# Kernel optimization log

Hardware: AMD Instinct MI355X
Metric: run time of the kernel (lower is better)

The kernel has to match this reference:

```python
import jax, jax.numpy as jnp
import numpy as np

NINP = 1024
NHID = 1024
BATCH = 16384
EPS = 1e-5


def _ln(x, g, b):
    mu = jnp.mean(x, axis=-1, keepdims=True)
    var = jnp.mean(jnp.square(x - mu), axis=-1, keepdims=True)
    return (x - mu) * jax.lax.rsqrt(var + EPS) * g + b


def setup_inputs() -> dict:
    key = jax.random.key(0)
    ks = jax.random.split(key, 12)
    s_i = 1.0 / np.sqrt(NINP)
    s_h = 1.0 / np.sqrt(NHID)
    return {
        "inp": jax.random.normal(ks[0], (BATCH, NINP), jnp.float32),
        "hidden": jax.random.normal(ks[1], (BATCH, NHID), jnp.float32),
        "W_i2gate": jax.random.uniform(ks[2], (3 * NHID, NINP), jnp.float32, -s_i, s_i),
        "b_i2gate": jnp.zeros((3 * NHID,), jnp.float32),
        "W_h2gate": jax.random.uniform(ks[3], (3 * NHID, NHID), jnp.float32, -s_h, s_h),
        "b_h2gate": jnp.zeros((3 * NHID,), jnp.float32),
        "W_i2i": jax.random.uniform(ks[4], (NHID, NINP), jnp.float32, -s_i, s_i),
        "b_i2i": jnp.zeros((NHID,), jnp.float32),
        "W_i2h": jax.random.uniform(ks[5], (NHID, NINP), jnp.float32, -s_i, s_i),
        "b_i2h": jnp.zeros((NHID,), jnp.float32),
        "W_h2h": jax.random.uniform(ks[6], (NHID, NHID), jnp.float32, -s_h, s_h),
        "b_h2h": jnp.zeros((NHID,), jnp.float32),
        "g_ig": jnp.ones((3 * NHID,), jnp.float32),
        "be_ig": jnp.zeros((3 * NHID,), jnp.float32),
        "g_hg": jnp.ones((3 * NHID,), jnp.float32),
        "be_hg": jnp.zeros((3 * NHID,), jnp.float32),
        "g_ii": jnp.ones((NHID,), jnp.float32),
        "be_ii": jnp.zeros((NHID,), jnp.float32),
        "g_ih": jnp.ones((NHID,), jnp.float32),
        "be_ih": jnp.zeros((NHID,), jnp.float32),
        "g_hh": jnp.ones((NHID,), jnp.float32),
        "be_hh": jnp.zeros((NHID,), jnp.float32),
    }


def reference(inp, hidden, W_i2gate, b_i2gate, W_h2gate, b_h2gate,
              W_i2i, b_i2i, W_i2h, b_i2h, W_h2h, b_h2h,
              g_ig, be_ig, g_hg, be_hg, g_ii, be_ii,
              g_ih, be_ih, g_hh, be_hh):
    gate = jax.nn.sigmoid(
        _ln(inp @ W_i2gate.T + b_i2gate, g_ig, be_ig)
        + _ln(hidden @ W_h2gate.T + b_h2gate, g_hg, be_hg))
    r, z, g = jnp.split(gate, 3, axis=-1)
    Hx = _ln(inp @ W_i2i.T + b_i2i, g_ii, be_ii)
    xh = _ln(inp @ W_i2h.T + b_i2h, g_ih, be_ih)
    hh = _ln(hidden @ W_h2h.T + b_h2h, g_hh, be_hh)
    hidden_m = jnp.tanh((1.0 - r) * xh + r * hh)
    return ((1.0 - z) * hidden + z * hidden_m) * (1.0 - g) + g * Hx
```

## Files before the change

kernel.cpp:

```cpp
#include <hip/hip_runtime.h>

typedef __bf16 bf16_t;
typedef bf16_t bf16x8 __attribute__((ext_vector_type(8)));
typedef bf16_t bf16x4 __attribute__((ext_vector_type(4)));
typedef float f32x4 __attribute__((ext_vector_type(4)));

#define BATCH 16384
#define KDIM  1024
#define NCOLS 9216

#define BMg 256
#define BNg 256
#define BKg 64
#define NTg (KDIM / BKg)
#define NBN (NCOLS / BNg)

__global__ __launch_bounds__(256)
void cast_all(const float* __restrict__ Wig, const float* __restrict__ Wii,
              const float* __restrict__ Wih, const float* __restrict__ Whg,
              const float* __restrict__ Whh,
              const float* __restrict__ big, const float* __restrict__ bii,
              const float* __restrict__ bih, const float* __restrict__ bhg,
              const float* __restrict__ bhh,
              const float* __restrict__ inp, const float* __restrict__ hid,
              bf16_t* __restrict__ Wcat, float* __restrict__ bcat,
              bf16_t* __restrict__ inpb, bf16_t* __restrict__ hidb,
              int nact_units, int ntot)
{
  int u = blockIdx.x * 256 + threadIdx.x;
  if (u >= ntot) return;

  if (u < 2359296) {
    const float* src; int off;
    if      (u < 786432)  { src = Wig; off = u; }
    else if (u < 1048576) { src = Wii; off = u - 786432; }
    else if (u < 1310720) { src = Wih; off = u - 1048576; }
    else if (u < 2097152) { src = Whg; off = u - 1310720; }
    else                  { src = Whh; off = u - 2097152; }
    float4 v = reinterpret_cast<const float4*>(src)[off];
    bf16x4 o;
    o[0] = (bf16_t)v.x; o[1] = (bf16_t)v.y; o[2] = (bf16_t)v.z; o[3] = (bf16_t)v.w;
    reinterpret_cast<bf16x4*>(Wcat)[u] = o;
  } else if (u < 2361600) {
    int bu = u - 2359296;
    int i = bu * 4;
    const float* src; int off;
    if      (i < 3072) { src = big; off = i; }
    else if (i < 4096) { src = bii; off = i - 3072; }
    else if (i < 5120) { src = bih; off = i - 4096; }
    else if (i < 8192) { src = bhg; off = i - 5120; }
    else               { src = bhh; off = i - 8192; }
    reinterpret_cast<float4*>(bcat)[bu] = *reinterpret_cast<const float4*>(src + off);
  } else {
    int au = u - 2361600;
    const float* src; bf16_t* dst; int off;
    if (au < nact_units) { src = inp; dst = inpb; off = au; }
    else                 { src = hid; dst = hidb; off = au - nact_units; }
    float4 v = reinterpret_cast<const float4*>(src)[off];
    bf16x4 o;
    o[0] = (bf16_t)v.x; o[1] = (bf16_t)v.y; o[2] = (bf16_t)v.z; o[3] = (bf16_t)v.w;
    reinterpret_cast<bf16x4*>(dst)[off] = o;
  }
}

__global__ __launch_bounds__(256)
void cast_acts(const float* __restrict__ inp, const float* __restrict__ hid,
               bf16_t* __restrict__ inpb, bf16_t* __restrict__ hidb, int n4) {
  int i = blockIdx.x * 256 + threadIdx.x;
  if (i >= 2 * n4) return;
  const float* src = (i < n4) ? inp : hid;
  bf16_t* dst = (i < n4) ? inpb : hidb;
  int off = (i < n4) ? i : i - n4;
  float4 v = reinterpret_cast<const float4*>(src)[off];
  bf16x4 o;
  o[0] = (bf16_t)v.x; o[1] = (bf16_t)v.y; o[2] = (bf16_t)v.z; o[3] = (bf16_t)v.w;
  reinterpret_cast<bf16x4*>(dst)[off] = o;
}

__global__ __launch_bounds__(512, 2)
void gemm_preln(const bf16_t* __restrict__ inpb, const bf16_t* __restrict__ hidb,
                const bf16_t* __restrict__ Wcat, const float* __restrict__ bcat,
                bf16_t* __restrict__ preLN, int nbm)
{
  __shared__ alignas(16) char lds_raw[131072];

  const int tid  = threadIdx.x;
  const int wid  = tid >> 6;
  const int lane = tid & 63;
  const int fr   = lane & 15;
  const int kg   = lane >> 4;
  const int wr   = wid >> 2;
  const int wc   = wid & 3;

  const int nwg = nbm * NBN;
  int orig = blockIdx.x;
  int q_ = nwg >> 3, r_ = nwg & 7, xcd = orig & 7, idx = orig >> 3;
  int wg = (xcd < r_ ? xcd * (q_ + 1) : r_ * (q_ + 1) + (xcd - r_) * q_) + idx;
  const int bm = wg / NBN, bn = wg % NBN;
  const int row0 = bm * BMg, col0 = bn * BNg;
  const bf16_t* __restrict__ act = (col0 < 5120) ? inpb : hidb;
  const bf16_t* __restrict__ wgt = Wcat + (size_t)col0 * KDIM;

  const int r_st  = tid >> 2;
  const int k8_st = (tid & 3) ^ ((r_st >> 1) & 3);
  const bf16_t* pA = act + (size_t)(row0 + r_st) * KDIM + k8_st * 8;
  const bf16_t* pB = wgt + (size_t)r_st * KDIM + k8_st * 8;

  auto stage_half = [&](int mat, int h, int T) {
    const bf16_t* s = (mat ? pB : pA) + ((size_t)h * 128) * KDIM + T * BKg;
    char* d = lds_raw + ((T & 1) << 16) + (mat << 15) + (h << 14) + (wid << 10);
    __builtin_amdgcn_global_load_lds(
        (const __attribute__((address_space(1))) unsigned int*)s,
        (__attribute__((address_space(3))) unsigned int*)d, 16, 0, 0);
    __builtin_amdgcn_global_load_lds(
        (const __attribute__((address_space(1))) unsigned int*)(s + 32),
        (__attribute__((address_space(3))) unsigned int*)(d + 8192), 16, 0, 0);
  };

  int offA[4][2], offB[2][2];
  #pragma unroll
  for (int m = 0; m < 4; ++m)
    #pragma unroll
    for (int ks = 0; ks < 2; ++ks) {
      const int rowA = wr * 64 + m * 16 + fr;
      offA[m][ks] = ks * 8192 + rowA * 64 + ((kg ^ ((rowA >> 1) & 3)) << 4);
    }
  #pragma unroll
  for (int n = 0; n < 2; ++n)
    #pragma unroll
    for (int ks = 0; ks < 2; ++ks) {
      const int rowB = wc * 32 + n * 16 + fr;
      offB[n][ks] = ks * 8192 + rowB * 64 + ((kg ^ ((rowB >> 1) & 3)) << 4);
    }

  f32x4 acc[2][4][2][2] = {};

  stage_half(0, 0, 0); stage_half(1, 0, 0);
  stage_half(0, 1, 0); stage_half(1, 1, 0);
  stage_half(0, 0, 1); stage_half(1, 0, 1);
  asm volatile("s_waitcnt vmcnt(4)" ::: "memory");
  __builtin_amdgcn_s_barrier();

  for (int T = 0; T < NTg; ++T) {
    const int bufo = (T & 1) << 16;
    bf16x8 a[4][2], b0[2][2], b1[2][2];

    #pragma unroll
    for (int m = 0; m < 4; ++m)
      #pragma unroll
      for (int ks = 0; ks < 2; ++ks)
        a[m][ks] = *(const bf16x8*)(lds_raw + bufo + offA[m][ks]);
    #pragma unroll
    for (int n = 0; n < 2; ++n)
      #pragma unroll
      for (int ks = 0; ks < 2; ++ks)
        b0[n][ks] = *(const bf16x8*)(lds_raw + bufo + 32768 + offB[n][ks]);
    if (T + 1 < NTg) stage_half(0, 1, T + 1);
    __builtin_amdgcn_s_barrier();
    asm volatile("s_waitcnt lgkmcnt(0)" ::: "memory");
    __builtin_amdgcn_sched_barrier(0);
    __builtin_amdgcn_s_setprio(1);
    #pragma unroll
    for (int m = 0; m < 4; ++m)
      #pragma unroll
      for (int n = 0; n < 2; ++n)
        #pragma unroll
        for (int ks = 0; ks < 2; ++ks)
          acc[0][m][0][n] = __builtin_amdgcn_mfma_f32_16x16x32_bf16(a[m][ks], b0[n][ks], acc[0][m][0][n], 0, 0, 0);
    __builtin_amdgcn_s_setprio(0);
    __builtin_amdgcn_s_barrier();

    #pragma unroll
    for (int n = 0; n < 2; ++n)
      #pragma unroll
      for (int ks = 0; ks < 2; ++ks)
        b1[n][ks] = *(const bf16x8*)(lds_raw + bufo + 32768 + 16384 + offB[n][ks]);
    if (T + 1 < NTg) stage_half(1, 1, T + 1);
    __builtin_amdgcn_s_barrier();
    asm volatile("s_waitcnt lgkmcnt(0)" ::: "memory");
    __builtin_amdgcn_sched_barrier(0);
    __builtin_amdgcn_s_setprio(1);
    #pragma unroll
    for (int m = 0; m < 4; ++m)
      #pragma unroll
      for (int n = 0; n < 2; ++n)
        #pragma unroll
        for (int ks = 0; ks < 2; ++ks)
          acc[0][m][1][n] = __builtin_amdgcn_mfma_f32_16x16x32_bf16(a[m][ks], b1[n][ks], acc[0][m][1][n], 0, 0, 0);
    __builtin_amdgcn_s_setprio(0);
    __builtin_amdgcn_s_barrier();

    #pragma unroll
    for (int m = 0; m < 4; ++m)
      #pragma unroll
      for (int ks = 0; ks < 2; ++ks)
        a[m][ks] = *(const bf16x8*)(lds_raw + bufo + 16384 + offA[m][ks]);
    if (T + 2 < NTg) stage_half(0, 0, T + 2);
    __builtin_amdgcn_s_barrier();
    asm volatile("s_waitcnt lgkmcnt(0)" ::: "memory");
    __builtin_amdgcn_sched_barrier(0);
    __builtin_amdgcn_s_setprio(1);
    #pragma unroll
    for (int m = 0; m < 4; ++m)
      #pragma unroll
      for (int n = 0; n < 2; ++n)
        #pragma unroll
        for (int ks = 0; ks < 2; ++ks)
          acc[1][m][1][n] = __builtin_amdgcn_mfma_f32_16x16x32_bf16(a[m][ks], b1[n][ks], acc[1][m][1][n], 0, 0, 0);
    __builtin_amdgcn_s_setprio(0);
    __builtin_amdgcn_s_barrier();

    if (T + 2 < NTg) stage_half(1, 0, T + 2);
    __builtin_amdgcn_s_barrier();
    __builtin_amdgcn_s_setprio(1);
    #pragma unroll
    for (int m = 0; m < 4; ++m)
      #pragma unroll
      for (int n = 0; n < 2; ++n)
        #pragma unroll
        for (int ks = 0; ks < 2; ++ks)
          acc[1][m][0][n] = __builtin_amdgcn_mfma_f32_16x16x32_bf16(a[m][ks], b0[n][ks], acc[1][m][0][n], 0, 0, 0);
    __builtin_amdgcn_s_setprio(0);

    if (T < NTg - 2) {
      asm volatile("s_waitcnt vmcnt(4)" ::: "memory");
      __builtin_amdgcn_s_barrier();
    } else if (T == NTg - 2) {
      asm volatile("s_waitcnt vmcnt(0)" ::: "memory");
      __builtin_amdgcn_s_barrier();
    }
  }

  #pragma unroll
  for (int qn_ = 0; qn_ < 2; ++qn_)
    #pragma unroll
    for (int n = 0; n < 2; ++n) {
      const int col = col0 + qn_ * 128 + wc * 32 + n * 16 + fr;
      const float bias = bcat[col];
      #pragma unroll
      for (int qm_ = 0; qm_ < 2; ++qm_)
        #pragma unroll
        for (int m = 0; m < 4; ++m) {
          const int rbase = row0 + qm_ * 128 + wr * 64 + m * 16 + kg * 4;
          #pragma unroll
          for (int j = 0; j < 4; ++j)
            preLN[(size_t)(rbase + j) * NCOLS + col] = (bf16_t)(acc[qm_][m][qn_][n][j] + bias);
        }
    }
}

__global__ __launch_bounds__(256)
void ln_combine(const bf16_t* __restrict__ preLN, const float* __restrict__ hidden,
                const float* __restrict__ g_ig, const float* __restrict__ be_ig,
                const float* __restrict__ g_hg, const float* __restrict__ be_hg,
                const float* __restrict__ g_ii, const float* __restrict__ be_ii,
                const float* __restrict__ g_ih, const float* __restrict__ be_ih,
                const float* __restrict__ g_hh, const float* __restrict__ be_hh,
                float* __restrict__ out, int crows)
{
  const int ln  = threadIdx.x & 63;
  const int row = blockIdx.x * 4 + (threadIdx.x >> 6);
  if (row >= crows) return;
  const bf16_t* __restrict__ src = preLN + (size_t)row * NCOLS;

  float s1[5] = {0.f,0.f,0.f,0.f,0.f}, s2[5] = {0.f,0.f,0.f,0.f,0.f};
  #pragma unroll
  for (int j = 0; j < 18; ++j) {
    const int sg = (j < 6) ? 0 : (j < 8) ? 1 : (j < 10) ? 2 : (j < 16) ? 3 : 4;
    bf16x8 v = *(const bf16x8*)(src + (size_t)(j * 64 + ln) * 8);
    #pragma unroll
    for (int t = 0; t < 8; ++t) {
      float f = (float)v[t];
      s1[sg] += f;
      s2[sg] += f * f;
    }
  }
  #pragma unroll
  for (int s = 0; s < 5; ++s)
    #pragma unroll
    for (int off = 32; off; off >>= 1) {
      s1[s] += __shfl_xor(s1[s], off);
      s2[s] += __shfl_xor(s2[s], off);
    }
  const float nn[5] = {3072.f, 1024.f, 1024.f, 3072.f, 1024.f};
  float mu[5], rs[5];
  #pragma unroll
  for (int s = 0; s < 5; ++s) {
    mu[s] = s1[s] / nn[s];
    rs[s] = rsqrtf(s2[s] / nn[s] - mu[s] * mu[s] + 1e-5f);
  }
  const float mu0 = mu[0], r0s = rs[0];
  const float mu1 = mu[1], r1s = rs[1];
  const float mu2 = mu[2], r2s = rs[2];
  const float mu3 = mu[3], r3s = rs[3];
  const float mu4 = mu[4], r4s = rs[4];

  const float* __restrict__ hrow = hidden + (size_t)row * 1024;
  float* __restrict__ orow = out + (size_t)row * 1024;
  #pragma unroll
  for (int p = 0; p < 4; ++p) {
    const int c = p * 256 + ln * 4;
    bf16x4 v_igr = *(const bf16x4*)&src[c];
    bf16x4 v_igz = *(const bf16x4*)&src[c + 1024];
    bf16x4 v_igg = *(const bf16x4*)&src[c + 2048];
    bf16x4 v_ii  = *(const bf16x4*)&src[c + 3072];
    bf16x4 v_ih  = *(const bf16x4*)&src[c + 4096];
    bf16x4 v_hgr = *(const bf16x4*)&src[c + 5120];
    bf16x4 v_hgz = *(const bf16x4*)&src[c + 6144];
    bf16x4 v_hgg = *(const bf16x4*)&src[c + 7168];
    bf16x4 v_hh  = *(const bf16x4*)&src[c + 8192];

    f32x4 Gr  = *(const f32x4*)&g_ig[c];        f32x4 Br  = *(const f32x4*)&be_ig[c];
    f32x4 Gz  = *(const f32x4*)&g_ig[c + 1024]; f32x4 Bz  = *(const f32x4*)&be_ig[c + 1024];
    f32x4 Gg  = *(const f32x4*)&g_ig[c + 2048]; f32x4 Bg  = *(const f32x4*)&be_ig[c + 2048];
    f32x4 Hr  = *(const f32x4*)&g_hg[c];        f32x4 Cr  = *(const f32x4*)&be_hg[c];
    f32x4 Hz  = *(const f32x4*)&g_hg[c + 1024]; f32x4 Cz  = *(const f32x4*)&be_hg[c + 1024];
    f32x4 Hg  = *(const f32x4*)&g_hg[c + 2048]; f32x4 Cg  = *(const f32x4*)&be_hg[c + 2048];
    f32x4 Gii = *(const f32x4*)&g_ii[c];        f32x4 Bii = *(const f32x4*)&be_ii[c];
    f32x4 Gih = *(const f32x4*)&g_ih[c];        f32x4 Bih = *(const f32x4*)&be_ih[c];
    f32x4 Ghh = *(const f32x4*)&g_hh[c];        f32x4 Bhh = *(const f32x4*)&be_hh[c];
    f32x4 hv  = *(const f32x4*)&hrow[c];

    f32x4 o;
    #pragma unroll
    for (int i = 0; i < 4; ++i) {
      float pr = ((float)v_igr[i] - mu0) * r0s * Gr[i] + Br[i]
               + ((float)v_hgr[i] - mu3) * r3s * Hr[i] + Cr[i];
      float pz = ((float)v_igz[i] - mu0) * r0s * Gz[i] + Bz[i]
               + ((float)v_hgz[i] - mu3) * r3s * Hz[i] + Cz[i];
      float pg = ((float)v_igg[i] - mu0) * r0s * Gg[i] + Bg[i]
               + ((float)v_hgg[i] - mu3) * r3s * Hg[i] + Cg[i];

      float rr = 1.f / (1.f + __expf(-pr));
      float zz = 1.f / (1.f + __expf(-pz));
      float gg = 1.f / (1.f + __expf(-pg));

      float Hx = ((float)v_ii[i] - mu1) * r1s * Gii[i] + Bii[i];
      float xh = ((float)v_ih[i] - mu2) * r2s * Gih[i] + Bih[i];
      float hh = ((float)v_hh[i] - mu4) * r4s * Ghh[i] + Bhh[i];

      float pre = (1.f - rr) * xh + rr * hh;
      float hm  = 1.f - 2.f / (1.f + __expf(2.f * pre));
      o[i] = ((1.f - zz) * hv[i] + zz * hm) * (1.f - gg) + gg * Hx;
    }
    *(f32x4*)&orow[c] = o;
  }
}

extern "C" void kernel_launch(void* const* d_in, const int* in_sizes, int n_in,
                              void* d_out, int out_size, void* d_ws, size_t ws_size,
                              hipStream_t stream) {
  const float* inp      = (const float*)d_in[0];
  const float* hidden   = (const float*)d_in[1];
  const float* W_i2gate = (const float*)d_in[2];
  const float* b_i2gate = (const float*)d_in[3];
  const float* W_h2gate = (const float*)d_in[4];
  const float* b_h2gate = (const float*)d_in[5];
  const float* W_i2i    = (const float*)d_in[6];
  const float* b_i2i    = (const float*)d_in[7];
  const float* W_i2h    = (const float*)d_in[8];
  const float* b_i2h    = (const float*)d_in[9];
  const float* W_h2h    = (const float*)d_in[10];
  const float* b_h2h    = (const float*)d_in[11];
  const float* g_ig  = (const float*)d_in[12];
  const float* be_ig = (const float*)d_in[13];
  const float* g_hg  = (const float*)d_in[14];
  const float* be_hg = (const float*)d_in[15];
  const float* g_ii  = (const float*)d_in[16];
  const float* be_ii = (const float*)d_in[17];
  const float* g_ih  = (const float*)d_in[18];
  const float* be_ih = (const float*)d_in[19];
  const float* g_hh  = (const float*)d_in[20];
  const float* be_hh = (const float*)d_in[21];
  float* out = (float*)d_out;

  const size_t WCAT_B  = (size_t)NCOLS * KDIM * 2;
  const size_t BCAT_B  = (size_t)NCOLS * 4;
  const size_t FIXED_B = WCAT_B + BCAT_B;
  const size_t PER_ROW = 2048 + 2048 + 18432;

  if (ws_size < FIXED_B + PER_ROW * 256) return;

  char* ws = (char*)d_ws;
  bf16_t* Wcat = (bf16_t*)ws;
  float*  bcat = (float*)(ws + WCAT_B);
  char*   dyn  = ws + FIXED_B;

  size_t max_rows = (ws_size - FIXED_B) / PER_ROW;
  int chunk = (int)((max_rows / 256) * 256);
  if (chunk > BATCH) chunk = BATCH;

  bf16_t* inpb  = (bf16_t*)dyn;
  bf16_t* hidb  = (bf16_t*)(dyn + (size_t)chunk * 2048);
  bf16_t* preLN = (bf16_t*)(dyn + (size_t)chunk * 4096);

  if (chunk == BATCH) {
    const int nact = BATCH * KDIM / 4;
    const int ntot = 2361600 + 2 * nact;
    cast_all<<<(ntot + 255) / 256, 256, 0, stream>>>(
        W_i2gate, W_i2i, W_i2h, W_h2gate, W_h2h,
        b_i2gate, b_i2i, b_i2h, b_h2gate, b_h2h,
        inp, hidden, Wcat, bcat, inpb, hidb, nact, ntot);

    int nbm = BATCH / BMg;
    gemm_preln<<<nbm * NBN, 512, 0, stream>>>(inpb, hidb, Wcat, bcat, preLN, nbm);

    ln_combine<<<BATCH / 4, 256, 0, stream>>>(preLN, hidden,
                                          g_ig, be_ig, g_hg, be_hg,
                                          g_ii, be_ii, g_ih, be_ih, g_hh, be_hh,
                                          out, BATCH);
  } else {
    const int ntot_w = 2361600;
    cast_all<<<(ntot_w + 255) / 256, 256, 0, stream>>>(
        W_i2gate, W_i2i, W_i2h, W_h2gate, W_h2h,
        b_i2gate, b_i2i, b_i2h, b_h2gate, b_h2h,
        nullptr, nullptr, Wcat, bcat, nullptr, nullptr, 0, ntot_w);

    for (int r0 = 0; r0 < BATCH; r0 += chunk) {
      int cr = BATCH - r0;
      if (cr > chunk) cr = chunk;
      int n4 = cr * KDIM / 4;
      cast_acts<<<(2 * n4 + 255) / 256, 256, 0, stream>>>(
          inp + (size_t)r0 * KDIM, hidden + (size_t)r0 * KDIM, inpb, hidb, n4);

      int nbm = cr / BMg;
      gemm_preln<<<nbm * NBN, 512, 0, stream>>>(inpb, hidb, Wcat, bcat, preLN, nbm);

      ln_combine<<<(cr + 3) / 4, 256, 0, stream>>>(preLN, hidden + (size_t)r0 * KDIM,
                                         g_ig, be_ig, g_hg, be_hg,
                                         g_ii, be_ii, g_ih, be_ih, g_hh, be_hh,
                                         out + (size_t)r0 * KDIM, cr);
    }
  }
}
```

Baseline: 518.9 us.

## Fuse LayerNorm partial statistics into GEMM epilogue and split combine

The GEMM epilogue now accumulates per-row sum and sum of squares of the bf16-rounded outputs over each wave's 32-column slice and writes partials to workspace. A small reduction kernel turns these into per-segment mean and rstd. A flatter combine kernel then reads preLN once per element instead of twice. This removes the stats pass over the 300MB preLN buffer, at the cost of shuffle work in the GEMM epilogue, partial-sum traffic and an extra launch.

```diff
diff --git a/kernel.cpp b/kernel.cpp
--- a/kernel.cpp
+++ b/kernel.cpp
@@ -4,6 +4,7 @@
 typedef bf16_t bf16x8 __attribute__((ext_vector_type(8)));
 typedef bf16_t bf16x4 __attribute__((ext_vector_type(4)));
 typedef float f32x4 __attribute__((ext_vector_type(4)));
+typedef float f32x8_t __attribute__((ext_vector_type(8)));
 
 #define BATCH 16384
 #define KDIM  1024
@@ -80,7 +81,8 @@
 __global__ __launch_bounds__(512, 2)
 void gemm_preln(const bf16_t* __restrict__ inpb, const bf16_t* __restrict__ hidb,
                 const bf16_t* __restrict__ Wcat, const float* __restrict__ bcat,
-                bf16_t* __restrict__ preLN, int nbm)
+                bf16_t* __restrict__ preLN,
+                float* __restrict__ part1, float* __restrict__ part2, int crows, int nbm)
 {
   __shared__ alignas(16) char lds_raw[131072];
 
@@ -231,120 +233,136 @@
     }
   }
 
-  #pragma unroll
-  for (int qn_ = 0; qn_ < 2; ++qn_)
-    #pragma unroll
-    for (int n = 0; n < 2; ++n) {
-      const int col = col0 + qn_ * 128 + wc * 32 + n * 16 + fr;
-      const float bias = bcat[col];
-      #pragma unroll
-      for (int qm_ = 0; qm_ < 2; ++qm_)
-        #pragma unroll
-        for (int m = 0; m < 4; ++m) {
-          const int rbase = row0 + qm_ * 128 + wr * 64 + m * 16 + kg * 4;
+  const int cb = bn * 4 + wc;
+  #pragma unroll
+  for (int qm_ = 0; qm_ < 2; ++qm_)
+    #pragma unroll
+    for (int m = 0; m < 4; ++m) {
+      float s1v[4] = {0.f, 0.f, 0.f, 0.f};
+      float s2v[4] = {0.f, 0.f, 0.f, 0.f};
+      const int rbase = row0 + qm_ * 128 + wr * 64 + m * 16 + kg * 4;
+      #pragma unroll
+      for (int qn_ = 0; qn_ < 2; ++qn_)
+        #pragma unroll
+        for (int n = 0; n < 2; ++n) {
+          const int col = col0 + qn_ * 128 + wc * 32 + n * 16 + fr;
+          const float bias = bcat[col];
           #pragma unroll
-          for (int j = 0; j < 4; ++j)
-            preLN[(size_t)(rbase + j) * NCOLS + col] = (bf16_t)(acc[qm_][m][qn_][n][j] + bias);
+          for (int j = 0; j < 4; ++j) {
+            bf16_t h = (bf16_t)(acc[qm_][m][qn_][n][j] + bias);
+            preLN[(size_t)(rbase + j) * NCOLS + col] = h;
+            float vr = (float)h;
+            s1v[j] += vr;
+            s2v[j] += vr * vr;
+          }
         }
+      #pragma unroll
+      for (int j = 0; j < 4; ++j) {
+        float a = s1v[j], b = s2v[j];
+        #pragma unroll
+        for (int off = 1; off < 16; off <<= 1) {
+          a += __shfl_xor(a, off);
+          b += __shfl_xor(b, off);
+        }
+        if (fr == 0) {
+          const int row = rbase + j;
+          part1[(size_t)cb * crows + row] = a;
+          part2[(size_t)cb * crows + row] = b;
+        }
+      }
     }
 }
 
 __global__ __launch_bounds__(256)
-void ln_combine(const bf16_t* __restrict__ preLN, const float* __restrict__ hidden,
-                const float* __restrict__ g_ig, const float* __restrict__ be_ig,
-                const float* __restrict__ g_hg, const float* __restrict__ be_hg,
-                const float* __restrict__ g_ii, const float* __restrict__ be_ii,
-                const float* __restrict__ g_ih, const float* __restrict__ be_ih,
-                const float* __restrict__ g_hh, const float* __restrict__ be_hh,
-                float* __restrict__ out, int crows)
+void stat_reduce(const float* __restrict__ part1, const float* __restrict__ part2,
+                 float* __restrict__ stats, int crows) {
+  int row = blockIdx.x * 256 + threadIdx.x;
+  if (row >= crows) return;
+  const int lo[5] = {0, 48, 64, 80, 128};
+  const int hi[5] = {48, 64, 80, 128, 144};
+  const float nn[5] = {3072.f, 1024.f, 1024.f, 3072.f, 1024.f};
+  #pragma unroll
+  for (int s = 0; s < 5; ++s) {
+    float t1 = 0.f, t2 = 0.f;
+    for (int c = lo[s]; c < hi[s]; ++c) {
+      t1 += part1[(size_t)c * crows + row];
+      t2 += part2[(size_t)c * crows + row];
+    }
+    float mu = t1 / nn[s];
+    stats[(size_t)row * 10 + s] = mu;
+    stats[(size_t)row * 10 + 5 + s] = rsqrtf(t2 / nn[s] - mu * mu + 1e-5f);
+  }
+}
+
+__device__ __forceinline__ f32x8_t ld8f(const float* __restrict__ p) {
+  f32x8_t r;
+  *(float4*)&r       = *(const float4*)p;
+  *((float4*)&r + 1) = *(const float4*)(p + 4);
+  return r;
+}
+__device__ __forceinline__ f32x8_t cvt8(bf16x8 v) {
+  f32x8_t r;
+  #pragma unroll
+  for (int i = 0; i < 8; ++i) r[i] = (float)v[i];
+  return r;
+}
+
+__global__ __launch_bounds__(256)
+void combine(const bf16_t* __restrict__ preLN, const float* __restrict__ stats,
+             const float* __restrict__ hidden,
+             const float* __restrict__ g_ig, const float* __restrict__ be_ig,
+             const float* __restrict__ g_hg, const float* __restrict__ be_hg,
+             const float* __restrict__ g_ii, const float* __restrict__ be_ii,
+             const float* __restrict__ g_ih, const float* __restrict__ be_ih,
+             const float* __restrict__ g_hh, const float* __restrict__ be_hh,
+             float* __restrict__ out, int crows)
 {
-  const int ln  = threadIdx.x & 63;
-  const int row = blockIdx.x * 4 + (threadIdx.x >> 6);
-  if (row >= crows) return;
-  const bf16_t* __restrict__ src = preLN + (size_t)row * NCOLS;
-
-  float s1[5] = {0.f,0.f,0.f,0.f,0.f}, s2[5] = {0.f,0.f,0.f,0.f,0.f};
-  #pragma unroll
-  for (int j = 0; j < 18; ++j) {
-    const int sg = (j < 6) ? 0 : (j < 8) ? 1 : (j < 10) ? 2 : (j < 16) ? 3 : 4;
-    bf16x8 v = *(const bf16x8*)(src + (size_t)(j * 64 + ln) * 8);
-    #pragma unroll
-    for (int t = 0; t < 8; ++t) {
-      float f = (float)v[t];
-      s1[sg] += f;
-      s2[sg] += f * f;
-    }
+  int id = blockIdx.x * 256 + threadIdx.x;
+  if (id >= crows * 128) return;
+  const int row = id >> 7;
+  const int c0  = (id & 127) * 8;
+
+  const float* __restrict__ st = stats + (size_t)row * 10;
+  const float mu0 = st[0], mu1 = st[1], mu2 = st[2], mu3 = st[3], mu4 = st[4];
+  const float r0 = st[5], r1 = st[6], r2 = st[7], r3 = st[8], r4 = st[9];
+
+  const bf16_t* __restrict__ src = preLN + (size_t)row * NCOLS + c0;
+  f32x8_t x_igr = cvt8(*(const bf16x8*)(src));
+  f32x8_t x_igz = cvt8(*(const bf16x8*)(src + 1024));
+  f32x8_t x_igg = cvt8(*(const bf16x8*)(src + 2048));
+  f32x8_t x_ii  = cvt8(*(const bf16x8*)(src + 3072));
+  f32x8_t x_ih  = cvt8(*(const bf16x8*)(src + 4096));
+  f32x8_t x_hgr = cvt8(*(const bf16x8*)(src + 5120));
+  f32x8_t x_hgz = cvt8(*(const bf16x8*)(src + 6144));
+  f32x8_t x_hgg = cvt8(*(const bf16x8*)(src + 7168));
+  f32x8_t x_hh  = cvt8(*(const bf16x8*)(src + 8192));
+
+  f32x8_t pr = (x_igr - mu0) * r0 * ld8f(g_ig + c0)        + ld8f(be_ig + c0)
+             + (x_hgr - mu3) * r3 * ld8f(g_hg + c0)        + ld8f(be_hg + c0);
+  f32x8_t pz = (x_igz - mu0) * r0 * ld8f(g_ig + c0 + 1024) + ld8f(be_ig + c0 + 1024)
+             + (x_hgz - mu3) * r3 * ld8f(g_hg + c0 + 1024) + ld8f(be_hg + c0 + 1024);
+  f32x8_t pg = (x_igg - mu0) * r0 * ld8f(g_ig + c0 + 2048) + ld8f(be_ig + c0 + 2048)
+             + (x_hgg - mu3) * r3 * ld8f(g_hg + c0 + 2048) + ld8f(be_hg + c0 + 2048);
+
+  f32x8_t Hx = (x_ii - mu1) * r1 * ld8f(g_ii + c0) + ld8f(be_ii + c0);
+  f32x8_t xh = (x_ih - mu2) * r2 * ld8f(g_ih + c0) + ld8f(be_ih + c0);
+  f32x8_t hh = (x_hh - mu4) * r4 * ld8f(g_hh + c0) + ld8f(be_hh + c0);
+
+  f32x8_t hv = ld8f(hidden + (size_t)row * 1024 + c0);
+
+  f32x8_t o;
+  #pragma unroll
+  for (int i = 0; i < 8; ++i) {
+    float rr = 1.f / (1.f + __expf(-pr[i]));
+    float zz = 1.f / (1.f + __expf(-pz[i]));
+    float gg = 1.f / (1.f + __expf(-pg[i]));
+    float pre = (1.f - rr) * xh[i] + rr * hh[i];
+    float hm  = 1.f - 2.f / (1.f + __expf(2.f * pre));
+    o[i] = ((1.f - zz) * hv[i] + zz * hm) * (1.f - gg) + gg * Hx[i];
   }
-  #pragma unroll
-  for (int s = 0; s < 5; ++s)
-    #pragma unroll
-    for (int off = 32; off; off >>= 1) {
-      s1[s] += __shfl_xor(s1[s], off);
-      s2[s] += __shfl_xor(s2[s], off);
-    }
-  const float nn[5] = {3072.f, 1024.f, 1024.f, 3072.f, 1024.f};
-  float mu[5], rs[5];
-  #pragma unroll
-  for (int s = 0; s < 5; ++s) {
-    mu[s] = s1[s] / nn[s];
-    rs[s] = rsqrtf(s2[s] / nn[s] - mu[s] * mu[s] + 1e-5f);
-  }
-  const float mu0 = mu[0], r0s = rs[0];
-  const float mu1 = mu[1], r1s = rs[1];
-  const float mu2 = mu[2], r2s = rs[2];
-  const float mu3 = mu[3], r3s = rs[3];
-  const float mu4 = mu[4], r4s = rs[4];
-
-  const float* __restrict__ hrow = hidden + (size_t)row * 1024;
-  float* __restrict__ orow = out + (size_t)row * 1024;
-  #pragma unroll
-  for (int p = 0; p < 4; ++p) {
-    const int c = p * 256 + ln * 4;
-    bf16x4 v_igr = *(const bf16x4*)&src[c];
-    bf16x4 v_igz = *(const bf16x4*)&src[c + 1024];
-    bf16x4 v_igg = *(const bf16x4*)&src[c + 2048];
-    bf16x4 v_ii  = *(const bf16x4*)&src[c + 3072];
-    bf16x4 v_ih  = *(const bf16x4*)&src[c + 4096];
-    bf16x4 v_hgr = *(const bf16x4*)&src[c + 5120];
-    bf16x4 v_hgz = *(const bf16x4*)&src[c + 6144];
-    bf16x4 v_hgg = *(const bf16x4*)&src[c + 7168];
-    bf16x4 v_hh  = *(const bf16x4*)&src[c + 8192];
-
-    f32x4 Gr  = *(const f32x4*)&g_ig[c];        f32x4 Br  = *(const f32x4*)&be_ig[c];
-    f32x4 Gz  = *(const f32x4*)&g_ig[c + 1024]; f32x4 Bz  = *(const f32x4*)&be_ig[c + 1024];
-    f32x4 Gg  = *(const f32x4*)&g_ig[c + 2048]; f32x4 Bg  = *(const f32x4*)&be_ig[c + 2048];
-    f32x4 Hr  = *(const f32x4*)&g_hg[c];        f32x4 Cr  = *(const f32x4*)&be_hg[c];
-    f32x4 Hz  = *(const f32x4*)&g_hg[c + 1024]; f32x4 Cz  = *(const f32x4*)&be_hg[c + 1024];
-    f32x4 Hg  = *(const f32x4*)&g_hg[c + 2048]; f32x4 Cg  = *(const f32x4*)&be_hg[c + 2048];
-    f32x4 Gii = *(const f32x4*)&g_ii[c];        f32x4 Bii = *(const f32x4*)&be_ii[c];
-    f32x4 Gih = *(const f32x4*)&g_ih[c];        f32x4 Bih = *(const f32x4*)&be_ih[c];
-    f32x4 Ghh = *(const f32x4*)&g_hh[c];        f32x4 Bhh = *(const f32x4*)&be_hh[c];
-    f32x4 hv  = *(const f32x4*)&hrow[c];
-
-    f32x4 o;
-    #pragma unroll
-    for (int i = 0; i < 4; ++i) {
-      float pr = ((float)v_igr[i] - mu0) * r0s * Gr[i] + Br[i]
-               + ((float)v_hgr[i] - mu3) * r3s * Hr[i] + Cr[i];
-      float pz = ((float)v_igz[i] - mu0) * r0s * Gz[i] + Bz[i]
-               + ((float)v_hgz[i] - mu3) * r3s * Hz[i] + Cz[i];
-      float pg = ((float)v_igg[i] - mu0) * r0s * Gg[i] + Bg[i]
-               + ((float)v_hgg[i] - mu3) * r3s * Hg[i] + Cg[i];
-
-      float rr = 1.f / (1.f + __expf(-pr));
-      float zz = 1.f / (1.f + __expf(-pz));
-      float gg = 1.f / (1.f + __expf(-pg));
-
-      float Hx = ((float)v_ii[i] - mu1) * r1s * Gii[i] + Bii[i];
-      float xh = ((float)v_ih[i] - mu2) * r2s * Gih[i] + Bih[i];
-      float hh = ((float)v_hh[i] - mu4) * r4s * Ghh[i] + Bhh[i];
-
-      float pre = (1.f - rr) * xh + rr * hh;
-      float hm  = 1.f - 2.f / (1.f + __expf(2.f * pre));
-      o[i] = ((1.f - zz) * hv[i] + zz * hm) * (1.f - gg) + gg * Hx;
-    }
-    *(f32x4*)&orow[c] = o;
-  }
+  float* __restrict__ dst = out + (size_t)row * 1024 + c0;
+  *(float4*)dst       = *(float4*)&o;
+  *((float4*)dst + 1) = *((float4*)&o + 1);
 }
 
 extern "C" void kernel_launch(void* const* d_in, const int* in_sizes, int n_in,
@@ -377,7 +395,7 @@
   const size_t WCAT_B  = (size_t)NCOLS * KDIM * 2;
   const size_t BCAT_B  = (size_t)NCOLS * 4;
   const size_t FIXED_B = WCAT_B + BCAT_B;
-  const size_t PER_ROW = 2048 + 2048 + 18432;
+  const size_t PER_ROW = 40 + 576 + 576 + 2048 + 2048 + 18432;
 
   if (ws_size < FIXED_B + PER_ROW * 256) return;
 
@@ -390,9 +408,12 @@
   int chunk = (int)((max_rows / 256) * 256);
   if (chunk > BATCH) chunk = BATCH;
 
-  bf16_t* inpb  = (bf16_t*)dyn;
-  bf16_t* hidb  = (bf16_t*)(dyn + (size_t)chunk * 2048);
-  bf16_t* preLN = (bf16_t*)(dyn + (size_t)chunk * 4096);
+  float*  stats = (float*)dyn;
+  float*  part1 = (float*)(dyn + (size_t)chunk * 40);
+  float*  part2 = (float*)(dyn + (size_t)chunk * (40 + 576));
+  bf16_t* inpb  = (bf16_t*)(dyn + (size_t)chunk * (40 + 1152));
+  bf16_t* hidb  = (bf16_t*)(dyn + (size_t)chunk * (40 + 1152 + 2048));
+  bf16_t* preLN = (bf16_t*)(dyn + (size_t)chunk * (40 + 1152 + 4096));
 
   if (chunk == BATCH) {
     const int nact = BATCH * KDIM / 4;
@@ -403,12 +424,15 @@
         inp, hidden, Wcat, bcat, inpb, hidb, nact, ntot);
 
     int nbm = BATCH / BMg;
-    gemm_preln<<<nbm * NBN, 512, 0, stream>>>(inpb, hidb, Wcat, bcat, preLN, nbm);
-
-    ln_combine<<<BATCH / 4, 256, 0, stream>>>(preLN, hidden,
-                                          g_ig, be_ig, g_hg, be_hg,
-                                          g_ii, be_ii, g_ih, be_ih, g_hh, be_hh,
-                                          out, BATCH);
+    gemm_preln<<<nbm * NBN, 512, 0, stream>>>(inpb, hidb, Wcat, bcat, preLN,
+                                              part1, part2, BATCH, nbm);
+
+    stat_reduce<<<(BATCH + 255) / 256, 256, 0, stream>>>(part1, part2, stats, BATCH);
+
+    combine<<<BATCH * 128 / 256, 256, 0, stream>>>(preLN, stats, hidden,
+                                       g_ig, be_ig, g_hg, be_hg,
+                                       g_ii, be_ii, g_ih, be_ih, g_hh, be_hh,
+                                       out, BATCH);
   } else {
     const int ntot_w = 2361600;
     cast_all<<<(ntot_w + 255) / 256, 256, 0, stream>>>(
@@ -424,9 +448,13 @@
           inp + (size_t)r0 * KDIM, hidden + (size_t)r0 * KDIM, inpb, hidb, n4);
 
       int nbm = cr / BMg;
-      gemm_preln<<<nbm * NBN, 512, 0, stream>>>(inpb, hidb, Wcat, bcat, preLN, nbm);
-
-      ln_combine<<<(cr + 3) / 4, 256, 0, stream>>>(preLN, hidden + (size_t)r0 * KDIM,
+      gemm_preln<<<nbm * NBN, 512, 0, stream>>>(inpb, hidb, Wcat, bcat, preLN,
+                                                part1, part2, cr, nbm);
+
+      stat_reduce<<<(cr + 255) / 256, 256, 0, stream>>>(part1, part2, stats, cr);
+
+      combine<<<cr * 128 / 256, 256, 0, stream>>>(preLN, stats,
+                                         hidden + (size_t)r0 * KDIM,
                                          g_ig, be_ig, g_hg, be_hg,
                                          g_ii, be_ii, g_ih, be_ih, g_hh, be_hh,
                                          out + (size_t)r0 * KDIM, cr);
```

After: 581.9 us. 12.1% more time.
